# Performance work log

Hardware: AMD Instinct MI355X
Metric: run time of the kernel (lower is better)

## Reference

```python
import jax, jax.numpy as jnp
import numpy as np

N_NODES = 100000
N_TYPES = 10
N_EDGES = 3200000
HIDDEN = 256
EMBED = 128
N_PAIRS = 100000


def setup_inputs() -> dict:
    key = jax.random.key(0)
    ks = jax.random.split(key, 16)
    node_type_ids = jax.random.randint(ks[0], (N_NODES,), 0, N_TYPES)
    rows = jnp.sort(jax.random.randint(ks[1], (N_EDGES,), 0, N_NODES))
    cols = jax.random.randint(ks[2], (N_EDGES,), 0, N_NODES)
    edge_vals = jax.random.uniform(ks[3], (N_EDGES,), dtype=jnp.float32)
    pairs = jax.random.randint(ks[4], (2, N_PAIRS), 0, N_NODES)
    s = 0.02
    node_emb = jax.random.normal(ks[5], (N_NODES, HIDDEN), jnp.float32) * s
    type_emb = jax.random.normal(ks[6], (N_TYPES, HIDDEN), jnp.float32) * s
    W1 = jax.random.normal(ks[7], (HIDDEN, HIDDEN), jnp.float32) * s
    b1 = jnp.zeros((HIDDEN,), jnp.float32)
    W2 = jax.random.normal(ks[8], (HIDDEN, EMBED), jnp.float32) * s
    b2 = jnp.zeros((EMBED,), jnp.float32)
    Wp1 = jax.random.normal(ks[9], (3 * EMBED, EMBED), jnp.float32) * s
    bp1 = jnp.zeros((EMBED,), jnp.float32)
    Wp2 = jax.random.normal(ks[10], (EMBED, 1), jnp.float32) * s
    bp2 = jnp.zeros((1,), jnp.float32)
    return {"node_type_ids": node_type_ids, "rows": rows, "cols": cols,
            "edge_vals": edge_vals, "pairs": pairs,
            "node_emb": node_emb, "type_emb": type_emb,
            "W1": W1, "b1": b1, "W2": W2, "b2": b2,
            "Wp1": Wp1, "bp1": bp1, "Wp2": Wp2, "bp2": bp2}


def reference(node_type_ids, rows, cols, edge_vals, pairs,
              node_emb, type_emb, W1, b1, W2, b2, Wp1, bp1, Wp2, bp2):
    N = node_emb.shape[0]

    def spmm(x):  # sparse.mm(adj, x): gather src feats, weight, scatter-add to rows
        return jax.ops.segment_sum(edge_vals[:, None] * x[cols], rows, num_segments=N)

    # encode (dropout p=0.0 -> identity)
    x = node_emb + type_emb[node_type_ids]            # [N, H]
    h = jax.nn.relu(spmm(x) @ W1 + b1)                # gcn1 + relu
    z = spmm(h) @ W2 + b2                             # gcn2 -> [N, E]

    # score
    src = z[pairs[0]]                                 # [P, E]
    dst = z[pairs[1]]
    feat = jnp.concatenate([src, dst, src * dst], axis=-1)  # [P, 3E]
    hp = jax.nn.relu(feat @ Wp1 + bp1)
    return (hp @ Wp2 + bp2).squeeze(-1)               # [P]
```

## Files before the change

kernel.cpp:

```cpp
#include <hip/hip_runtime.h>
#include <hip/hip_bf16.h>

#define N_NODES 100000
#define N_TYPES 10
#define N_EDGES 3200000
#define HIDDEN 256
#define EMBED 128
#define N_PAIRS 100000

typedef _Float16 half2v __attribute__((ext_vector_type(2)));
typedef _Float16 half4v __attribute__((ext_vector_type(4)));
typedef _Float16 half8v __attribute__((ext_vector_type(8)));
typedef float floatx2 __attribute__((ext_vector_type(2)));
typedef float floatx4 __attribute__((ext_vector_type(4)));

#define GLOBAL_AS __attribute__((address_space(1)))
#define LDS_AS __attribute__((address_space(3)))

#define X8_SCALE 16.0f
#define X8_INV  (1.0f / 16.0f)
#define G8_SCALE 64.0f
#define G8_INV  (1.0f / 64.0f)

static __device__ __forceinline__ void async_copy16(const void* g, void* lds) {
    __builtin_amdgcn_global_load_lds((const GLOBAL_AS unsigned int*)g,
                                     (LDS_AS unsigned int*)(void*)lds, 16, 0, 0);
}

__global__ void build_rowptr_k(const int* __restrict__ rows, int* __restrict__ rp,
                               int n_nodes, int n_edges) {
    int n = blockIdx.x * blockDim.x + threadIdx.x;
    if (n > n_nodes) return;
    int lo = 0, hi = n_edges;
    while (lo < hi) {
        int mid = (lo + hi) >> 1;
        if (rows[mid] < n) lo = mid + 1; else hi = mid;
    }
    rp[n] = lo;
}

__global__ void build_x8_k(const float* __restrict__ node_emb,
                           const float* __restrict__ type_emb,
                           const int* __restrict__ ntype,
                           unsigned char* __restrict__ x8) {
    int idx = blockIdx.x * blockDim.x + threadIdx.x;
    int n  = idx >> 6;
    if (n >= N_NODES) return;
    int f4 = (idx & 63) * 4;
    int t = ntype[n];
    float4 a = *(const float4*)&node_emb[(size_t)n * HIDDEN + f4];
    float4 b = *(const float4*)&type_emb[(size_t)t * HIDDEN + f4];
    int w = __builtin_amdgcn_cvt_pk_fp8_f32((a.x + b.x) * X8_SCALE,
                                            (a.y + b.y) * X8_SCALE, 0, false);
    w     = __builtin_amdgcn_cvt_pk_fp8_f32((a.z + b.z) * X8_SCALE,
                                            (a.w + b.w) * X8_SCALE, w, true);
    *(int*)&x8[(size_t)n * HIDDEN + f4] = w;
}

__global__ void transpose_w_k(const float* __restrict__ W, _Float16* __restrict__ Wt,
                              int K, int N) {
    int idx = blockIdx.x * blockDim.x + threadIdx.x;
    if (idx >= K * N) return;
    int k = idx & 255;
    int n = idx >> 8;
    Wt[idx] = (_Float16)W[(size_t)k * N + n];
}

__global__ void transpose_wp1_k(const float* __restrict__ W, _Float16* __restrict__ Wt) {
    int k = threadIdx.x;
    int n = blockIdx.x;
    Wt[n * 384 + k] = (_Float16)W[(size_t)k * EMBED + n];
}

__global__ void spmm1_k(const int* __restrict__ rp, const int* __restrict__ cols,
                        const float* __restrict__ vals,
                        const unsigned char* __restrict__ x8,
                        _Float16* __restrict__ s1) {
    int wave = threadIdx.x >> 6, lane = threadIdx.x & 63;
    int n = blockIdx.x * 4 + wave;
    int e0 = rp[n], e1 = rp[n + 1];
    int fo = lane * 4;
    float a0 = 0.f, a1 = 0.f, a2 = 0.f, a3 = 0.f;
    int e = e0;
    for (; e + 16 <= e1; e += 16) {
        int c[16]; float v[16];
#pragma unroll
        for (int i = 0; i < 16; ++i) { c[i] = cols[e + i]; v[i] = vals[e + i]; }
        int w[16];
#pragma unroll
        for (int i = 0; i < 16; ++i)
            w[i] = *(const int*)&x8[(size_t)c[i] * HIDDEN + fo];
#pragma unroll
        for (int i = 0; i < 16; ++i) {
            floatx2 lo = __builtin_amdgcn_cvt_pk_f32_fp8(w[i], false);
            floatx2 hi = __builtin_amdgcn_cvt_pk_f32_fp8(w[i], true);
            a0 += v[i] * lo.x; a1 += v[i] * lo.y;
            a2 += v[i] * hi.x; a3 += v[i] * hi.y;
        }
    }
    for (; e + 4 <= e1; e += 4) {
        int c[4]; float v[4];
#pragma unroll
        for (int i = 0; i < 4; ++i) { c[i] = cols[e + i]; v[i] = vals[e + i]; }
        int w[4];
#pragma unroll
        for (int i = 0; i < 4; ++i)
            w[i] = *(const int*)&x8[(size_t)c[i] * HIDDEN + fo];
#pragma unroll
        for (int i = 0; i < 4; ++i) {
            floatx2 lo = __builtin_amdgcn_cvt_pk_f32_fp8(w[i], false);
            floatx2 hi = __builtin_amdgcn_cvt_pk_f32_fp8(w[i], true);
            a0 += v[i] * lo.x; a1 += v[i] * lo.y;
            a2 += v[i] * hi.x; a3 += v[i] * hi.y;
        }
    }
    for (; e < e1; ++e) {
        int c0 = cols[e]; float v0 = vals[e];
        int w0 = *(const int*)&x8[(size_t)c0 * HIDDEN + fo];
        floatx2 lo = __builtin_amdgcn_cvt_pk_f32_fp8(w0, false);
        floatx2 hi = __builtin_amdgcn_cvt_pk_f32_fp8(w0, true);
        a0 += v0 * lo.x; a1 += v0 * lo.y;
        a2 += v0 * hi.x; a3 += v0 * hi.y;
    }
    half4v o;
    o.x = (_Float16)(a0 * X8_INV); o.y = (_Float16)(a1 * X8_INV);
    o.z = (_Float16)(a2 * X8_INV); o.w = (_Float16)(a3 * X8_INV);
    *(half4v*)&s1[(size_t)n * HIDDEN + fo] = o;
}

__global__ void spmm2_k(const int* __restrict__ rp, const int* __restrict__ cols,
                        const float* __restrict__ vals,
                        const unsigned char* __restrict__ g8,
                        const float* __restrict__ b2, _Float16* __restrict__ z16) {
    int wave = threadIdx.x >> 6, lane = threadIdx.x & 63;
    int n = blockIdx.x * 4 + wave;
    int e0 = rp[n], e1 = rp[n + 1];
    int fo = lane * 2;
    float ax = 0.f, ay = 0.f;
    int e = e0;
    for (; e + 16 <= e1; e += 16) {
        int c[16]; float v[16];
#pragma unroll
        for (int i = 0; i < 16; ++i) { c[i] = cols[e + i]; v[i] = vals[e + i]; }
        unsigned short w[16];
#pragma unroll
        for (int i = 0; i < 16; ++i)
            w[i] = *(const unsigned short*)&g8[(size_t)c[i] * EMBED + fo];
#pragma unroll
        for (int i = 0; i < 16; ++i) {
            floatx2 d = __builtin_amdgcn_cvt_pk_f32_fp8((int)w[i], false);
            ax += v[i] * d.x;
            ay += v[i] * d.y;
        }
    }
    for (; e + 4 <= e1; e += 4) {
        int c[4]; float v[4];
#pragma unroll
        for (int i = 0; i < 4; ++i) { c[i] = cols[e + i]; v[i] = vals[e + i]; }
        unsigned short w[4];
#pragma unroll
        for (int i = 0; i < 4; ++i)
            w[i] = *(const unsigned short*)&g8[(size_t)c[i] * EMBED + fo];
#pragma unroll
        for (int i = 0; i < 4; ++i) {
            floatx2 d = __builtin_amdgcn_cvt_pk_f32_fp8((int)w[i], false);
            ax += v[i] * d.x;
            ay += v[i] * d.y;
        }
    }
    for (; e < e1; ++e) {
        int c0 = cols[e]; float v0 = vals[e];
        unsigned short w0 = *(const unsigned short*)&g8[(size_t)c0 * EMBED + fo];
        floatx2 d = __builtin_amdgcn_cvt_pk_f32_fp8((int)w0, false);
        ax += v0 * d.x;
        ay += v0 * d.y;
    }
    half2v o;
    o.x = (_Float16)(ax * G8_INV + b2[fo]);
    o.y = (_Float16)(ay * G8_INV + b2[fo + 1]);
    *(half2v*)&z16[(size_t)n * EMBED + fo] = o;
}

template <bool RELU, bool BIAS, bool FP8OUT>
__global__ void gemm16_k(const _Float16* __restrict__ A,
                         const _Float16* __restrict__ Bt,
                         const float* __restrict__ bias,
                         void* __restrict__ Cout,
                         int M, int N) {
    const int K = 256;
    __shared__ _Float16 As[128 * 32];
    __shared__ _Float16 Bs[128 * 32];

    int t = threadIdx.x;
    int lane = t & 63;
    int wave = t >> 6;
    int quad = lane >> 4;
    int m16 = lane & 15;
    int wr = wave >> 1, wc = wave & 1;
    int m0 = blockIdx.x * 128;
    int n0 = blockIdx.y * 128;

    int srow = t >> 2;
    int skoff = (t & 3) * 8;

    floatx4 acc[4][4];
#pragma unroll
    for (int i = 0; i < 4; ++i)
#pragma unroll
        for (int j = 0; j < 4; ++j)
            acc[i][j] = (floatx4)0.f;

    for (int k0 = 0; k0 < K; k0 += 32) {
        int ra0 = m0 + srow;       if (ra0 >= M) ra0 = M - 1;
        int ra1 = m0 + srow + 64;  if (ra1 >= M) ra1 = M - 1;
        async_copy16(&A[(size_t)ra0 * K + k0 + skoff], &As[srow * 32 + skoff]);
        async_copy16(&A[(size_t)ra1 * K + k0 + skoff], &As[(srow + 64) * 32 + skoff]);
        async_copy16(&Bt[(size_t)(n0 + srow) * K + k0 + skoff], &Bs[srow * 32 + skoff]);
        async_copy16(&Bt[(size_t)(n0 + srow + 64) * K + k0 + skoff], &Bs[(srow + 64) * 32 + skoff]);
        __syncthreads();

        half8v aF[4], bF[4];
#pragma unroll
        for (int i = 0; i < 4; ++i)
            aF[i] = *(const half8v*)&As[(wr * 64 + i * 16 + m16) * 32 + quad * 8];
#pragma unroll
        for (int j = 0; j < 4; ++j)
            bF[j] = *(const half8v*)&Bs[(wc * 64 + j * 16 + m16) * 32 + quad * 8];
#pragma unroll
        for (int i = 0; i < 4; ++i)
#pragma unroll
            for (int j = 0; j < 4; ++j)
                acc[i][j] = __builtin_amdgcn_mfma_f32_16x16x32_f16(aF[i], bF[j], acc[i][j], 0, 0, 0);
        __syncthreads();
    }

#pragma unroll
    for (int i = 0; i < 4; ++i) {
#pragma unroll
        for (int j = 0; j < 4; ++j) {
            int gr = m0 + wr * 64 + i * 16 + quad * 4;
            int gc = n0 + wc * 64 + j * 16 + m16;
            float bv = BIAS ? bias[gc] : 0.f;
#pragma unroll
            for (int r = 0; r < 4; ++r) {
                int row = gr + r;
                if (row < M) {
                    float v = acc[i][j][r] + bv;
                    if (RELU) v = v > 0.f ? v : 0.f;
                    if (FP8OUT) {
                        float sv = v * G8_SCALE;
                        int w = __builtin_amdgcn_cvt_pk_fp8_f32(sv, sv, 0, false);
                        ((unsigned char*)Cout)[(size_t)row * N + gc] = (unsigned char)(w & 0xFF);
                    } else {
                        ((_Float16*)Cout)[(size_t)row * N + gc] = (_Float16)v;
                    }
                }
            }
        }
    }
}

__global__ __launch_bounds__(256) void scorer_mfma_k(
        const _Float16* __restrict__ z16, const int* __restrict__ pairs,
        const _Float16* __restrict__ Wp1t, const float* __restrict__ bp1,
        const float* __restrict__ Wp2, const float* __restrict__ bp2,
        float* __restrict__ out, int P) {
    __shared__ _Float16 Fs[128][136];
    __shared__ _Float16 Ws[128][136];
    __shared__ int sidx[128], didx[128];
    __shared__ float red[128][2];

    int t  = threadIdx.x;
    int p0 = blockIdx.x * 128;

    if (t < 128) {
        int p = p0 + t;
        if (p >= P) p = P - 1;
        sidx[t] = pairs[p];
        didx[t] = pairs[P + p];
    }
    __syncthreads();

    int lane = t & 63, wave = t >> 6;
    int quad = lane >> 4, m16 = lane & 15;
    int wr = wave >> 1, wc = wave & 1;

    floatx4 acc[4][4];
#pragma unroll
    for (int i = 0; i < 4; ++i)
#pragma unroll
        for (int j = 0; j < 4; ++j)
            acc[i][j] = (floatx4)0.f;

    int pr = t & 127;
    int kh = (t >> 7) * 64;

    for (int r = 0; r < 3; ++r) {
        {
            const _Float16* zs = &z16[(size_t)sidx[pr] * EMBED + kh];
            const _Float16* zd = &z16[(size_t)didx[pr] * EMBED + kh];
            half8v f[8];
            if (r == 0) {
#pragma unroll
                for (int i = 0; i < 8; ++i) f[i] = *(const half8v*)&zs[i * 8];
            } else if (r == 1) {
#pragma unroll
                for (int i = 0; i < 8; ++i) f[i] = *(const half8v*)&zd[i * 8];
            } else {
#pragma unroll
                for (int i = 0; i < 8; ++i) {
                    half8v a = *(const half8v*)&zs[i * 8];
                    half8v b = *(const half8v*)&zd[i * 8];
                    f[i] = a * b;
                }
            }
#pragma unroll
            for (int i = 0; i < 8; ++i)
                *(half8v*)&Fs[pr][kh + i * 8] = f[i];
        }
        {
            const _Float16* wsrc = &Wp1t[(size_t)pr * 384 + r * 128 + kh];
#pragma unroll
            for (int i = 0; i < 8; ++i)
                *(half8v*)&Ws[pr][kh + i * 8] = *(const half8v*)&wsrc[i * 8];
        }
        __syncthreads();

#pragma unroll
        for (int k0 = 0; k0 < 128; k0 += 32) {
            half8v aF[4], bF[4];
#pragma unroll
            for (int i = 0; i < 4; ++i)
                aF[i] = *(const half8v*)&Fs[wr * 64 + i * 16 + m16][k0 + quad * 8];
#pragma unroll
            for (int j = 0; j < 4; ++j)
                bF[j] = *(const half8v*)&Ws[wc * 64 + j * 16 + m16][k0 + quad * 8];
#pragma unroll
            for (int i = 0; i < 4; ++i)
#pragma unroll
                for (int j = 0; j < 4; ++j)
                    acc[i][j] = __builtin_amdgcn_mfma_f32_16x16x32_f16(aF[i], bF[j], acc[i][j], 0, 0, 0);
        }
        __syncthreads();
    }

    float w2v[4], b1v[4];
#pragma unroll
    for (int j = 0; j < 4; ++j) {
        int col = wc * 64 + j * 16 + m16;
        w2v[j] = Wp2[col];
        b1v[j] = bp1[col];
    }
#pragma unroll
    for (int i = 0; i < 4; ++i) {
#pragma unroll
        for (int rr = 0; rr < 4; ++rr) {
            float partial = 0.f;
#pragma unroll
            for (int j = 0; j < 4; ++j) {
                float v = acc[i][j][rr] + b1v[j];
                v = v > 0.f ? v : 0.f;
                partial += v * w2v[j];
            }
#pragma unroll
            for (int off = 1; off < 16; off <<= 1)
                partial += __shfl_xor(partial, off, 64);
            if (m16 == 0)
                red[wr * 64 + i * 16 + quad * 4 + rr][wc] = partial;
        }
    }
    __syncthreads();
    if (t < 128) {
        int p = p0 + t;
        if (p < P) out[p] = red[t][0] + red[t][1] + bp2[0];
    }
}

extern "C" void kernel_launch(void* const* d_in, const int* in_sizes, int n_in,
                              void* d_out, int out_size, void* d_ws, size_t ws_size,
                              hipStream_t stream) {
    const int*   node_type_ids = (const int*)d_in[0];
    const int*   rows          = (const int*)d_in[1];
    const int*   cols          = (const int*)d_in[2];
    const float* edge_vals     = (const float*)d_in[3];
    const int*   pairs         = (const int*)d_in[4];
    const float* node_emb      = (const float*)d_in[5];
    const float* type_emb      = (const float*)d_in[6];
    const float* W1            = (const float*)d_in[7];
    const float* b1            = (const float*)d_in[8];
    const float* W2            = (const float*)d_in[9];
    const float* b2            = (const float*)d_in[10];
    const float* Wp1           = (const float*)d_in[11];
    const float* bp1           = (const float*)d_in[12];
    const float* Wp2           = (const float*)d_in[13];
    const float* bp2           = (const float*)d_in[14];
    float* out = (float*)d_out;

    const size_t MB = 1ull << 20;
    char* ws = (char*)d_ws;
    int*      rp   = (int*)(ws);
    unsigned char* x8 = (unsigned char*)(ws + 4 * MB);
    _Float16* s1   = (_Float16*)(ws + 56 * MB);
    _Float16* h16  = (_Float16*)(ws + 108 * MB);
    unsigned char* g8 = (unsigned char*)(ws + 160 * MB);
    _Float16* z16  = (_Float16*)(ws + 186 * MB);
    _Float16* W1t  = (_Float16*)(ws + 212 * MB);
    _Float16* W2t  = (_Float16*)(ws + 213 * MB);
    _Float16* Wp1t = (_Float16*)(ws + 214 * MB);

    build_rowptr_k<<<(N_NODES + 256) / 256, 256, 0, stream>>>(rows, rp, N_NODES, N_EDGES);
    build_x8_k<<<(N_NODES * 64 + 255) / 256, 256, 0, stream>>>(node_emb, type_emb,
                                                               node_type_ids, x8);
    transpose_w_k<<<(HIDDEN * HIDDEN + 255) / 256, 256, 0, stream>>>(W1, W1t, HIDDEN, HIDDEN);
    transpose_w_k<<<(HIDDEN * EMBED + 255) / 256, 256, 0, stream>>>(W2, W2t, HIDDEN, EMBED);
    transpose_wp1_k<<<EMBED, 3 * EMBED, 0, stream>>>(Wp1, Wp1t);

    spmm1_k<<<N_NODES / 4, 256, 0, stream>>>(rp, cols, edge_vals, x8, s1);

    {
        dim3 grid((N_NODES + 127) / 128, HIDDEN / 128);
        gemm16_k<true, true, false><<<grid, 256, 0, stream>>>(s1, W1t, b1, h16, N_NODES, HIDDEN);
    }

    {
        dim3 grid((N_NODES + 127) / 128, EMBED / 128);
        gemm16_k<false, false, true><<<grid, 256, 0, stream>>>(h16, W2t, nullptr, g8, N_NODES, EMBED);
    }

    spmm2_k<<<N_NODES / 4, 256, 0, stream>>>(rp, cols, edge_vals, g8, b2, z16);

    scorer_mfma_k<<<(N_PAIRS + 127) / 128, 256, 0, stream>>>(z16, pairs, Wp1t, bp1,
                                                             Wp2, bp2, out, N_PAIRS);
}
```

Baseline: 510.2 us.

## Use 16-lane row groups with wide gathers in SpMM and a full-width GEMM1

Both SpMM kernels now assign a 16-lane group to each node, so every lane gathers 16 or 8 contiguous fp8 bytes in one vector load instead of 4 or 2 bytes. This gives fewer, wider memory transactions per edge and four nodes per wave. The edge loop is processed in predicated chunks of 8 with no scalar tail loops. GEMM1 becomes a single 512-thread kernel covering all 256 output columns, so each A tile is loaded once rather than once per column block. The cost is higher register pressure, occupancy set by launch bounds, and uneven edge counts across the four nodes sharing a wave.

Result: faster. 481.2 us (-5.7%).

```diff
diff --git a/kernel.cpp b/kernel.cpp
--- a/kernel.cpp
+++ b/kernel.cpp
@@ -13,6 +13,8 @@
 typedef _Float16 half8v __attribute__((ext_vector_type(8)));
 typedef float floatx2 __attribute__((ext_vector_type(2)));
 typedef float floatx4 __attribute__((ext_vector_type(4)));
+typedef unsigned int uintx2 __attribute__((ext_vector_type(2)));
+typedef unsigned int uintx4 __attribute__((ext_vector_type(4)));
 
 #define GLOBAL_AS __attribute__((address_space(1)))
 #define LDS_AS __attribute__((address_space(3)))
@@ -72,121 +74,182 @@
     Wt[n * 384 + k] = (_Float16)W[(size_t)k * EMBED + n];
 }
 
-__global__ void spmm1_k(const int* __restrict__ rp, const int* __restrict__ cols,
-                        const float* __restrict__ vals,
-                        const unsigned char* __restrict__ x8,
-                        _Float16* __restrict__ s1) {
-    int wave = threadIdx.x >> 6, lane = threadIdx.x & 63;
-    int n = blockIdx.x * 4 + wave;
+__global__ __launch_bounds__(256, 5) void spmm1_k(
+        const int* __restrict__ rp, const int* __restrict__ cols,
+        const float* __restrict__ vals,
+        const unsigned char* __restrict__ x8,
+        _Float16* __restrict__ s1) {
+    int t = threadIdx.x;
+    int wave = t >> 6, lane = t & 63;
+    int g = lane >> 4, s = lane & 15;
+    int n = blockIdx.x * 16 + wave * 4 + g;
     int e0 = rp[n], e1 = rp[n + 1];
-    int fo = lane * 4;
-    float a0 = 0.f, a1 = 0.f, a2 = 0.f, a3 = 0.f;
-    int e = e0;
-    for (; e + 16 <= e1; e += 16) {
-        int c[16]; float v[16];
-#pragma unroll
-        for (int i = 0; i < 16; ++i) { c[i] = cols[e + i]; v[i] = vals[e + i]; }
-        int w[16];
-#pragma unroll
-        for (int i = 0; i < 16; ++i)
-            w[i] = *(const int*)&x8[(size_t)c[i] * HIDDEN + fo];
-#pragma unroll
-        for (int i = 0; i < 16; ++i) {
-            floatx2 lo = __builtin_amdgcn_cvt_pk_f32_fp8(w[i], false);
-            floatx2 hi = __builtin_amdgcn_cvt_pk_f32_fp8(w[i], true);
-            a0 += v[i] * lo.x; a1 += v[i] * lo.y;
-            a2 += v[i] * hi.x; a3 += v[i] * hi.y;
-        }
-    }
-    for (; e + 4 <= e1; e += 4) {
-        int c[4]; float v[4];
-#pragma unroll
-        for (int i = 0; i < 4; ++i) { c[i] = cols[e + i]; v[i] = vals[e + i]; }
-        int w[4];
+    int fo = s * 16;
+    const unsigned char* xbase = x8 + fo;
+    float acc[16];
+#pragma unroll
+    for (int j = 0; j < 16; ++j) acc[j] = 0.f;
+
+    for (int e = e0; e < e1; e += 8) {
+        int c[8]; float v[8];
+#pragma unroll
+        for (int i = 0; i < 8; ++i) {
+            int idx = e + i;
+            bool ok = idx < e1;
+            idx = ok ? idx : e;
+            c[i] = cols[idx];
+            v[i] = ok ? vals[idx] : 0.f;
+        }
+        uintx4 w[8];
+#pragma unroll
+        for (int i = 0; i < 8; ++i)
+            w[i] = *(const uintx4*)&xbase[(size_t)c[i] * HIDDEN];
+#pragma unroll
+        for (int i = 0; i < 8; ++i) {
+#pragma unroll
+            for (int q = 0; q < 4; ++q) {
+                int wq = (int)w[i][q];
+                floatx2 lo = __builtin_amdgcn_cvt_pk_f32_fp8(wq, false);
+                floatx2 hi = __builtin_amdgcn_cvt_pk_f32_fp8(wq, true);
+                acc[q * 4 + 0] += v[i] * lo.x;
+                acc[q * 4 + 1] += v[i] * lo.y;
+                acc[q * 4 + 2] += v[i] * hi.x;
+                acc[q * 4 + 3] += v[i] * hi.y;
+            }
+        }
+    }
+    half8v o0, o1;
+#pragma unroll
+    for (int j = 0; j < 8; ++j) {
+        o0[j] = (_Float16)(acc[j] * X8_INV);
+        o1[j] = (_Float16)(acc[8 + j] * X8_INV);
+    }
+    *(half8v*)&s1[(size_t)n * HIDDEN + fo]     = o0;
+    *(half8v*)&s1[(size_t)n * HIDDEN + fo + 8] = o1;
+}
+
+__global__ __launch_bounds__(256, 6) void spmm2_k(
+        const int* __restrict__ rp, const int* __restrict__ cols,
+        const float* __restrict__ vals,
+        const unsigned char* __restrict__ g8,
+        const float* __restrict__ b2, _Float16* __restrict__ z16) {
+    int t = threadIdx.x;
+    int wave = t >> 6, lane = t & 63;
+    int g = lane >> 4, s = lane & 15;
+    int n = blockIdx.x * 16 + wave * 4 + g;
+    int e0 = rp[n], e1 = rp[n + 1];
+    int fo = s * 8;
+    const unsigned char* gbase = g8 + fo;
+    float acc[8];
+#pragma unroll
+    for (int j = 0; j < 8; ++j) acc[j] = 0.f;
+
+    for (int e = e0; e < e1; e += 8) {
+        int c[8]; float v[8];
+#pragma unroll
+        for (int i = 0; i < 8; ++i) {
+            int idx = e + i;
+            bool ok = idx < e1;
+            idx = ok ? idx : e;
+            c[i] = cols[idx];
+            v[i] = ok ? vals[idx] : 0.f;
+        }
+        uintx2 w[8];
+#pragma unroll
+        for (int i = 0; i < 8; ++i)
+            w[i] = *(const uintx2*)&gbase[(size_t)c[i] * EMBED];
+#pragma unroll
+        for (int i = 0; i < 8; ++i) {
+#pragma unroll
+            for (int q = 0; q < 2; ++q) {
+                int wq = (int)w[i][q];
+                floatx2 lo = __builtin_amdgcn_cvt_pk_f32_fp8(wq, false);
+                floatx2 hi = __builtin_amdgcn_cvt_pk_f32_fp8(wq, true);
+                acc[q * 4 + 0] += v[i] * lo.x;
+                acc[q * 4 + 1] += v[i] * lo.y;
+                acc[q * 4 + 2] += v[i] * hi.x;
+                acc[q * 4 + 3] += v[i] * hi.y;
+            }
+        }
+    }
+    half8v o;
+#pragma unroll
+    for (int j = 0; j < 8; ++j)
+        o[j] = (_Float16)(acc[j] * G8_INV + b2[fo + j]);
+    *(half8v*)&z16[(size_t)n * EMBED + fo] = o;
+}
+
+__global__ __launch_bounds__(512) void gemm_wide_k(
+        const _Float16* __restrict__ A, const _Float16* __restrict__ Bt,
+        const float* __restrict__ bias, _Float16* __restrict__ C, int M) {
+    const int K = 256;
+    __shared__ _Float16 As[128 * 32];
+    __shared__ _Float16 Bs[256 * 32];
+
+    int t = threadIdx.x;
+    int lane = t & 63;
+    int wave = t >> 6;
+    int quad = lane >> 4;
+    int m16 = lane & 15;
+    int wr = wave >> 2, wc = wave & 3;
+    int m0 = blockIdx.x * 128;
+
+    int srow = t >> 2;
+    int skoff = (t & 3) * 8;
+
+    floatx4 acc[4][4];
+#pragma unroll
+    for (int i = 0; i < 4; ++i)
+#pragma unroll
+        for (int j = 0; j < 4; ++j)
+            acc[i][j] = (floatx4)0.f;
+
+    for (int k0 = 0; k0 < K; k0 += 32) {
+        int ra = m0 + srow; if (ra >= M) ra = M - 1;
+        async_copy16(&A[(size_t)ra * K + k0 + skoff], &As[srow * 32 + skoff]);
+        async_copy16(&Bt[(size_t)srow * K + k0 + skoff], &Bs[srow * 32 + skoff]);
+        async_copy16(&Bt[(size_t)(srow + 128) * K + k0 + skoff], &Bs[(srow + 128) * 32 + skoff]);
+        __syncthreads();
+
+        half8v aF[4], bF[4];
 #pragma unroll
         for (int i = 0; i < 4; ++i)
-            w[i] = *(const int*)&x8[(size_t)c[i] * HIDDEN + fo];
-#pragma unroll
-        for (int i = 0; i < 4; ++i) {
-            floatx2 lo = __builtin_amdgcn_cvt_pk_f32_fp8(w[i], false);
-            floatx2 hi = __builtin_amdgcn_cvt_pk_f32_fp8(w[i], true);
-            a0 += v[i] * lo.x; a1 += v[i] * lo.y;
-            a2 += v[i] * hi.x; a3 += v[i] * hi.y;
-        }
-    }
-    for (; e < e1; ++e) {
-        int c0 = cols[e]; float v0 = vals[e];
-        int w0 = *(const int*)&x8[(size_t)c0 * HIDDEN + fo];
-        floatx2 lo = __builtin_amdgcn_cvt_pk_f32_fp8(w0, false);
-        floatx2 hi = __builtin_amdgcn_cvt_pk_f32_fp8(w0, true);
-        a0 += v0 * lo.x; a1 += v0 * lo.y;
-        a2 += v0 * hi.x; a3 += v0 * hi.y;
-    }
-    half4v o;
-    o.x = (_Float16)(a0 * X8_INV); o.y = (_Float16)(a1 * X8_INV);
-    o.z = (_Float16)(a2 * X8_INV); o.w = (_Float16)(a3 * X8_INV);
-    *(half4v*)&s1[(size_t)n * HIDDEN + fo] = o;
-}
-
-__global__ void spmm2_k(const int* __restrict__ rp, const int* __restrict__ cols,
-                        const float* __restrict__ vals,
-                        const unsigned char* __restrict__ g8,
-                        const float* __restrict__ b2, _Float16* __restrict__ z16) {
-    int wave = threadIdx.x >> 6, lane = threadIdx.x & 63;
-    int n = blockIdx.x * 4 + wave;
-    int e0 = rp[n], e1 = rp[n + 1];
-    int fo = lane * 2;
-    float ax = 0.f, ay = 0.f;
-    int e = e0;
-    for (; e + 16 <= e1; e += 16) {
-        int c[16]; float v[16];
-#pragma unroll
-        for (int i = 0; i < 16; ++i) { c[i] = cols[e + i]; v[i] = vals[e + i]; }
-        unsigned short w[16];
-#pragma unroll
-        for (int i = 0; i < 16; ++i)
-            w[i] = *(const unsigned short*)&g8[(size_t)c[i] * EMBED + fo];
-#pragma unroll
-        for (int i = 0; i < 16; ++i) {
-            floatx2 d = __builtin_amdgcn_cvt_pk_f32_fp8((int)w[i], false);
-            ax += v[i] * d.x;
-            ay += v[i] * d.y;
-        }
-    }
-    for (; e + 4 <= e1; e += 4) {
-        int c[4]; float v[4];
-#pragma unroll
-        for (int i = 0; i < 4; ++i) { c[i] = cols[e + i]; v[i] = vals[e + i]; }
-        unsigned short w[4];
+            aF[i] = *(const half8v*)&As[(wr * 64 + i * 16 + m16) * 32 + quad * 8];
+#pragma unroll
+        for (int j = 0; j < 4; ++j)
+            bF[j] = *(const half8v*)&Bs[(wc * 64 + j * 16 + m16) * 32 + quad * 8];
 #pragma unroll
         for (int i = 0; i < 4; ++i)
-            w[i] = *(const unsigned short*)&g8[(size_t)c[i] * EMBED + fo];
-#pragma unroll
-        for (int i = 0; i < 4; ++i) {
-            floatx2 d = __builtin_amdgcn_cvt_pk_f32_fp8((int)w[i], false);
-            ax += v[i] * d.x;
-            ay += v[i] * d.y;
-        }
-    }
-    for (; e < e1; ++e) {
-        int c0 = cols[e]; float v0 = vals[e];
-        unsigned short w0 = *(const unsigned short*)&g8[(size_t)c0 * EMBED + fo];
-        floatx2 d = __builtin_amdgcn_cvt_pk_f32_fp8((int)w0, false);
-        ax += v0 * d.x;
-        ay += v0 * d.y;
-    }
-    half2v o;
-    o.x = (_Float16)(ax * G8_INV + b2[fo]);
-    o.y = (_Float16)(ay * G8_INV + b2[fo + 1]);
-    *(half2v*)&z16[(size_t)n * EMBED + fo] = o;
-}
-
-template <bool RELU, bool BIAS, bool FP8OUT>
-__global__ void gemm16_k(const _Float16* __restrict__ A,
-                         const _Float16* __restrict__ Bt,
-                         const float* __restrict__ bias,
-                         void* __restrict__ Cout,
-                         int M, int N) {
+#pragma unroll
+            for (int j = 0; j < 4; ++j)
+                acc[i][j] = __builtin_amdgcn_mfma_f32_16x16x32_f16(aF[i], bF[j], acc[i][j], 0, 0, 0);
+        __syncthreads();
+    }
+
+#pragma unroll
+    for (int i = 0; i < 4; ++i) {
+#pragma unroll
+        for (int j = 0; j < 4; ++j) {
+            int gr = m0 + wr * 64 + i * 16 + quad * 4;
+            int gc = wc * 64 + j * 16 + m16;
+            float bv = bias[gc];
+#pragma unroll
+            for (int r = 0; r < 4; ++r) {
+                int row = gr + r;
+                if (row < M) {
+                    float v = acc[i][j][r] + bv;
+                    v = v > 0.f ? v : 0.f;
+                    C[(size_t)row * 256 + gc] = (_Float16)v;
+                }
+            }
+        }
+    }
+}
+
+__global__ void gemm2_k(const _Float16* __restrict__ A,
+                        const _Float16* __restrict__ Bt,
+                        unsigned char* __restrict__ Cout,
+                        int M, int N) {
     const int K = 256;
     __shared__ _Float16 As[128 * 32];
     __shared__ _Float16 Bs[128 * 32];
@@ -240,20 +303,13 @@
         for (int j = 0; j < 4; ++j) {
             int gr = m0 + wr * 64 + i * 16 + quad * 4;
             int gc = n0 + wc * 64 + j * 16 + m16;
-            float bv = BIAS ? bias[gc] : 0.f;
 #pragma unroll
             for (int r = 0; r < 4; ++r) {
                 int row = gr + r;
                 if (row < M) {
-                    float v = acc[i][j][r] + bv;
-                    if (RELU) v = v > 0.f ? v : 0.f;
-                    if (FP8OUT) {
-                        float sv = v * G8_SCALE;
-                        int w = __builtin_amdgcn_cvt_pk_fp8_f32(sv, sv, 0, false);
-                        ((unsigned char*)Cout)[(size_t)row * N + gc] = (unsigned char)(w & 0xFF);
-                    } else {
-                        ((_Float16*)Cout)[(size_t)row * N + gc] = (_Float16)v;
-                    }
+                    float sv = acc[i][j][r] * G8_SCALE;
+                    int w = __builtin_amdgcn_cvt_pk_fp8_f32(sv, sv, 0, false);
+                    Cout[(size_t)row * N + gc] = (unsigned char)(w & 0xFF);
                 }
             }
         }
@@ -415,19 +471,16 @@
     transpose_w_k<<<(HIDDEN * EMBED + 255) / 256, 256, 0, stream>>>(W2, W2t, HIDDEN, EMBED);
     transpose_wp1_k<<<EMBED, 3 * EMBED, 0, stream>>>(Wp1, Wp1t);
 
-    spmm1_k<<<N_NODES / 4, 256, 0, stream>>>(rp, cols, edge_vals, x8, s1);
-
-    {
-        dim3 grid((N_NODES + 127) / 128, HIDDEN / 128);
-        gemm16_k<true, true, false><<<grid, 256, 0, stream>>>(s1, W1t, b1, h16, N_NODES, HIDDEN);
-    }
+    spmm1_k<<<N_NODES / 16, 256, 0, stream>>>(rp, cols, edge_vals, x8, s1);
+
+    gemm_wide_k<<<(N_NODES + 127) / 128, 512, 0, stream>>>(s1, W1t, b1, h16, N_NODES);
 
     {
         dim3 grid((N_NODES + 127) / 128, EMBED / 128);
-        gemm16_k<false, false, true><<<grid, 256, 0, stream>>>(h16, W2t, nullptr, g8, N_NODES, EMBED);
-    }
-
-    spmm2_k<<<N_NODES / 4, 256, 0, stream>>>(rp, cols, edge_vals, g8, b2, z16);
+        gemm2_k<<<grid, 256, 0, stream>>>(h16, W2t, g8, N_NODES, EMBED);
+    }
+
+    spmm2_k<<<N_NODES / 16, 256, 0, stream>>>(rp, cols, edge_vals, g8, b2, z16);
 
     scorer_mfma_k<<<(N_PAIRS + 127) / 128, 256, 0, stream>>>(z16, pairs, Wp1t, bp1,
                                                              Wp2, bp2, out, N_PAIRS);
```
